# Performance work log

Measured on AMD Instinct MI355X. Metric: run time of the kernel, lower is better.

The kernel has to match this reference:

```python
import jax, jax.numpy as jnp
import numpy as np

VOCAB = 10000
HIDDEN = 256
BATCH = 32
SEQ = 256


def setup_inputs() -> dict:
    key = jax.random.key(0)
    ks = jax.random.split(key, 7)
    s = 1.0 / np.sqrt(HIDDEN)  # torch nn.RNN/Linear init scale
    return {
        "inputs": jax.random.randint(ks[0], (BATCH, SEQ), 0, VOCAB),
        "state": jnp.zeros((1, BATCH, HIDDEN), dtype=jnp.float32),
        "W_ih": jax.random.uniform(ks[1], (HIDDEN, VOCAB), jnp.float32, -s, s),
        "b_ih": jax.random.uniform(ks[2], (HIDDEN,), jnp.float32, -s, s),
        "W_hh": jax.random.uniform(ks[3], (HIDDEN, HIDDEN), jnp.float32, -s, s),
        "b_hh": jax.random.uniform(ks[4], (HIDDEN,), jnp.float32, -s, s),
        "W_out": jax.random.uniform(ks[5], (VOCAB, HIDDEN), jnp.float32, -s, s),
        "b_out": jax.random.uniform(ks[6], (VOCAB,), jnp.float32, -s, s),
    }


def reference(inputs, state, W_ih, b_ih, W_hh, b_hh, W_out, b_out):
    # one_hot(inputs.T) @ W_ih.T is exactly a row-gather of W_ih.T (one-hot
    # entries are exactly 1.0), so gather gives bitwise-identical math.
    # xproj: (seq, batch, hidden)
    xproj = W_ih.T[inputs.T] + b_ih + b_hh

    def step(h, x_t):
        h = jnp.tanh(x_t + h @ W_hh.T)  # (batch, hidden)
        return h, h

    h_last, Y = jax.lax.scan(step, state[0], xproj)  # Y: (seq, batch, hidden)
    logits = Y.reshape(-1, HIDDEN) @ W_out.T + b_out  # (seq*batch, vocab)
    return logits, h_last[None]
```

## Files before the change

kernel.cpp:

```cpp
#include <hip/hip_runtime.h>

#define VOCAB 10000
#define HIDDEN 256
#define BATCH 32
#define SEQ 256
#define NPAD 10112
#define NTILES 79
#define MTILES 64
#define LOGITS_ELEMS 81920000LL

typedef __attribute__((ext_vector_type(8))) short short8;
typedef __attribute__((ext_vector_type(4))) float f32x4;

static __device__ __forceinline__ unsigned short f32_to_bf16(float f) {
    unsigned u = __float_as_uint(f);
    u += 0x7fffu + ((u >> 16) & 1u);
    return (unsigned short)(u >> 16);
}

__global__ __launch_bounds__(256) void transpose_wih(const float* __restrict__ W_ih,
                                                     float* __restrict__ W_ihT) {
    __shared__ float tile[64][65];
    const int v0   = (blockIdx.x >> 2) * 64;
    const int h0   = (blockIdx.x & 3) * 64;
    const int lane = threadIdx.x & 63;
    const int wv   = threadIdx.x >> 6;

#pragma unroll
    for (int i = 0; i < 16; ++i) {
        const int row = i * 4 + wv;
        const int v   = v0 + lane;
        if (v < VOCAB)
            tile[row][lane] = W_ih[(long)(h0 + row) * VOCAB + v];
    }
    __syncthreads();
#pragma unroll
    for (int i = 0; i < 16; ++i) {
        const int vrow = i * 4 + wv;
        const int v    = v0 + vrow;
        if (v < VOCAB)
            W_ihT[(long)v * HIDDEN + h0 + lane] = tile[lane][vrow];
    }
}

__global__ __launch_bounds__(256) void prep_wout(const float* __restrict__ W_out,
                                                 unsigned short* __restrict__ Wb) {
    const int n = blockIdx.x;
    const int k = threadIdx.x;
    float v = (n < VOCAB) ? W_out[(long)n * HIDDEN + k] : 0.f;
    Wb[(long)n * HIDDEN + k] = f32_to_bf16(v);
}

__global__ __launch_bounds__(512, 2) void scan_kernel(
        const int*   __restrict__ inputs,
        const float* __restrict__ state,
        const float* __restrict__ W_hh,
        const float* __restrict__ b_ih,
        const float* __restrict__ b_hh,
        const float* __restrict__ W_ihT,
        unsigned short* __restrict__ Ybf,
        float* __restrict__ hout)
{
    __shared__ float hbuf[HIDDEN];
    __shared__ float psum[4 * HIDDEN];

    const int b  = blockIdx.x;
    const int t  = threadIdx.x;
    const int jj = t & 63;
    const int q  = (t >> 6) & 3;
    const int h2 = t >> 8;

    float w[2][64];
#pragma unroll
    for (int r = 0; r < 2; ++r) {
        const float* src = W_hh + (jj + 64 * (2 * h2 + r)) * HIDDEN + 64 * q;
#pragma unroll
        for (int k4 = 0; k4 < 16; ++k4) {
            const float4 v = *(const float4*)(src + 4 * k4);
            w[r][4 * k4 + 0] = v.x;
            w[r][4 * k4 + 1] = v.y;
            w[r][4 * k4 + 2] = v.z;
            w[r][4 * k4 + 3] = v.w;
        }
    }

    float biasv = 0.f, xcur = 0.f;
    if (t < HIDDEN) {
        biasv   = b_ih[t] + b_hh[t];
        hbuf[t] = state[b * HIDDEN + t];
        const int tok0 = inputs[b * SEQ];
        xcur = W_ihT[(long)tok0 * HIDDEN + t];
    }
    __syncthreads();

    for (int step = 0; step < SEQ; ++step) {
        float xnext = 0.f;
        if (t < HIDDEN && step + 1 < SEQ) {
            const int tokn = inputs[b * SEQ + step + 1];
            xnext = W_ihT[(long)tokn * HIDDEN + t];
        }

        float a00 = 0.f, a01 = 0.f, a10 = 0.f, a11 = 0.f;
#pragma unroll
        for (int k4 = 0; k4 < 8; ++k4) {
            const float4 hv = *(const float4*)&hbuf[64 * q + 4 * k4];
            a00 = fmaf(w[0][4 * k4 + 0], hv.x, a00);
            a00 = fmaf(w[0][4 * k4 + 1], hv.y, a00);
            a00 = fmaf(w[0][4 * k4 + 2], hv.z, a00);
            a00 = fmaf(w[0][4 * k4 + 3], hv.w, a00);
            a10 = fmaf(w[1][4 * k4 + 0], hv.x, a10);
            a10 = fmaf(w[1][4 * k4 + 1], hv.y, a10);
            a10 = fmaf(w[1][4 * k4 + 2], hv.z, a10);
            a10 = fmaf(w[1][4 * k4 + 3], hv.w, a10);
        }
#pragma unroll
        for (int k4 = 8; k4 < 16; ++k4) {
            const float4 hv = *(const float4*)&hbuf[64 * q + 4 * k4];
            a01 = fmaf(w[0][4 * k4 + 0], hv.x, a01);
            a01 = fmaf(w[0][4 * k4 + 1], hv.y, a01);
            a01 = fmaf(w[0][4 * k4 + 2], hv.z, a01);
            a01 = fmaf(w[0][4 * k4 + 3], hv.w, a01);
            a11 = fmaf(w[1][4 * k4 + 0], hv.x, a11);
            a11 = fmaf(w[1][4 * k4 + 1], hv.y, a11);
            a11 = fmaf(w[1][4 * k4 + 2], hv.z, a11);
            a11 = fmaf(w[1][4 * k4 + 3], hv.w, a11);
        }
        psum[q * HIDDEN + jj + 64 * (2 * h2 + 0)] = a00 + a01;
        psum[q * HIDDEN + jj + 64 * (2 * h2 + 1)] = a10 + a11;
        __syncthreads();

        if (t < HIDDEN) {
            const float s = psum[t] + psum[HIDDEN + t]
                          + psum[2 * HIDDEN + t] + psum[3 * HIDDEN + t];
            const float hnew = tanhf(s + xcur + biasv);
            hbuf[t] = hnew;
            Ybf[((long)step * BATCH + b) * HIDDEN + t] = f32_to_bf16(hnew);
            xcur = xnext;
        }
        __syncthreads();
    }

    if (t < HIDDEN) hout[b * HIDDEN + t] = hbuf[t];
}

__global__ __launch_bounds__(256) void gemm_kernel(
        const unsigned short* __restrict__ A,
        const unsigned short* __restrict__ B,
        const float* __restrict__ bias,
        float* __restrict__ C)
{
    __shared__ __align__(16) unsigned short lA[2][128 * 64];
    __shared__ __align__(16) unsigned short lB[2][128 * 64];

    const int t     = threadIdx.x;
    const int bid   = blockIdx.x;
    const int ntile = bid % NTILES;
    const int mtile = bid / NTILES;
    const long m0   = (long)mtile * 128;
    const long n0   = (long)ntile * 128;
    const int lane  = t & 63;
    const int wave  = t >> 6;
    const int wm    = (wave & 1) * 64;
    const int wn    = (wave >> 1) * 64;
    const int l15   = lane & 15;
    const int quad  = lane >> 4;

    const f32x4 zero = {0.f, 0.f, 0.f, 0.f};
    f32x4 acc[4][4];
#pragma unroll
    for (int i = 0; i < 4; ++i)
#pragma unroll
        for (int j = 0; j < 4; ++j)
            acc[i][j] = zero;

    auto stage = [&](int kb, int buf) {
#pragma unroll
        for (int it = 0; it < 4; ++it) {
            const int c   = it * 256 + t;
            const int row = c >> 3;
            const int sk8 = (c & 7) ^ (row & 7);
            const unsigned short* ga = A + (m0 + row) * HIDDEN + kb * 64 + sk8 * 8;
            const unsigned short* gb = B + (n0 + row) * HIDDEN + kb * 64 + sk8 * 8;
            __builtin_amdgcn_global_load_lds(
                (const __attribute__((address_space(1))) void*)ga,
                (__attribute__((address_space(3))) void*)(&lA[buf][c * 8]), 16, 0, 0);
            __builtin_amdgcn_global_load_lds(
                (const __attribute__((address_space(1))) void*)gb,
                (__attribute__((address_space(3))) void*)(&lB[buf][c * 8]), 16, 0, 0);
        }
    };

    stage(0, 0);
    __syncthreads();

#pragma unroll
    for (int kb = 0; kb < 4; ++kb) {
        if (kb < 3) stage(kb + 1, (kb + 1) & 1);
        const unsigned short* bufA = lA[kb & 1];
        const unsigned short* bufB = lB[kb & 1];
#pragma unroll
        for (int ki = 0; ki < 2; ++ki) {
            short8 af[4], bf[4];
#pragma unroll
            for (int i = 0; i < 4; ++i) {
                const int ra = wm + 16 * i + l15;
                af[i] = *(const short8*)
                    &bufA[ra * 64 + (((ki * 4 + quad) ^ (ra & 7)) * 8)];
                const int rb = wn + 16 * i + l15;
                bf[i] = *(const short8*)
                    &bufB[rb * 64 + (((ki * 4 + quad) ^ (rb & 7)) * 8)];
            }
#pragma unroll
            for (int i = 0; i < 4; ++i)
#pragma unroll
                for (int j = 0; j < 4; ++j)
                    acc[i][j] = __builtin_amdgcn_mfma_f32_16x16x32_bf16(
                        af[i], bf[j], acc[i][j], 0, 0, 0);
        }
        if (kb < 3) __syncthreads();
    }

#pragma unroll
    for (int j = 0; j < 4; ++j) {
        const long col = n0 + wn + 16 * j + l15;
        if (col < VOCAB) {
            const float bv = bias[col];
#pragma unroll
            for (int i = 0; i < 4; ++i) {
                const long row = m0 + wm + 16 * i + quad * 4;
                float* Cp = C + row * VOCAB + col;
#pragma unroll
                for (int r = 0; r < 4; ++r)
                    __builtin_nontemporal_store(acc[i][j][r] + bv,
                                                Cp + (long)r * VOCAB);
            }
        }
    }
}

extern "C" void kernel_launch(void* const* d_in, const int* in_sizes, int n_in,
                              void* d_out, int out_size, void* d_ws, size_t ws_size,
                              hipStream_t stream) {
    const int*   inputs = (const int*)  d_in[0];
    const float* state  = (const float*)d_in[1];
    const float* W_ih   = (const float*)d_in[2];
    const float* b_ih   = (const float*)d_in[3];
    const float* W_hh   = (const float*)d_in[4];
    const float* b_hh   = (const float*)d_in[5];
    const float* W_out  = (const float*)d_in[6];
    const float* b_out  = (const float*)d_in[7];
    float* out = (float*)d_out;

    char* ws = (char*)d_ws;
    float*          W_ihT = (float*)ws;
    unsigned short* Wb    = (unsigned short*)(ws + 10240000);
    unsigned short* Ybf   = (unsigned short*)(ws + 15417344);

    transpose_wih<<<157 * 4, 256, 0, stream>>>(W_ih, W_ihT);
    prep_wout<<<NPAD, 256, 0, stream>>>(W_out, Wb);
    scan_kernel<<<BATCH, 512, 0, stream>>>(inputs, state, W_hh, b_ih, b_hh,
                                           W_ihT, Ybf, out + LOGITS_ELEMS);
    gemm_kernel<<<MTILES * NTILES, 256, 0, stream>>>(Ybf, Wb, b_out, out);
}
```

Before: 603.5 us.

## Restructure RNN scan to one barrier per step and merge prep kernels

The scan kernel now assigns each hidden unit to a pair of half-wave lanes that each cover half of K. The two partial sums are combined with a cross-lane shuffle instead of an LDS partial-sum reduction, and the hidden state is double-buffered, so each timestep needs one barrier instead of two. The two weight-prep kernels (W_ih transpose and W_out bf16 conversion) are fused into a single launch to remove one kernel launch. The trade-offs are 128 weight registers per thread and redundant tanh/x loads across lane pairs.

Result: slower. 828.7 us (+37.3%).

```diff
diff --git a/kernel.cpp b/kernel.cpp
--- a/kernel.cpp
+++ b/kernel.cpp
@@ -8,6 +8,8 @@
 #define NTILES 79
 #define MTILES 64
 #define LOGITS_ELEMS 81920000LL
+#define TR_BLOCKS 628
+#define PREP_BLOCKS 707
 
 typedef __attribute__((ext_vector_type(8))) short short8;
 typedef __attribute__((ext_vector_type(4))) float f32x4;
@@ -18,37 +20,41 @@
     return (unsigned short)(u >> 16);
 }
 
-__global__ __launch_bounds__(256) void transpose_wih(const float* __restrict__ W_ih,
-                                                     float* __restrict__ W_ihT) {
+__global__ __launch_bounds__(256) void prep_kernel(const float* __restrict__ W_ih,
+                                                   float* __restrict__ W_ihT,
+                                                   const float* __restrict__ W_out,
+                                                   unsigned short* __restrict__ Wb) {
     __shared__ float tile[64][65];
-    const int v0   = (blockIdx.x >> 2) * 64;
-    const int h0   = (blockIdx.x & 3) * 64;
-    const int lane = threadIdx.x & 63;
-    const int wv   = threadIdx.x >> 6;
-
-#pragma unroll
-    for (int i = 0; i < 16; ++i) {
-        const int row = i * 4 + wv;
-        const int v   = v0 + lane;
-        if (v < VOCAB)
-            tile[row][lane] = W_ih[(long)(h0 + row) * VOCAB + v];
-    }
-    __syncthreads();
-#pragma unroll
-    for (int i = 0; i < 16; ++i) {
-        const int vrow = i * 4 + wv;
-        const int v    = v0 + vrow;
-        if (v < VOCAB)
-            W_ihT[(long)v * HIDDEN + h0 + lane] = tile[lane][vrow];
-    }
-}
-
-__global__ __launch_bounds__(256) void prep_wout(const float* __restrict__ W_out,
-                                                 unsigned short* __restrict__ Wb) {
-    const int n = blockIdx.x;
-    const int k = threadIdx.x;
-    float v = (n < VOCAB) ? W_out[(long)n * HIDDEN + k] : 0.f;
-    Wb[(long)n * HIDDEN + k] = f32_to_bf16(v);
+    const int t = threadIdx.x;
+    if (blockIdx.x < TR_BLOCKS) {
+        const int v0   = (blockIdx.x >> 2) * 64;
+        const int h0   = (blockIdx.x & 3) * 64;
+        const int lane = t & 63;
+        const int wv   = t >> 6;
+#pragma unroll
+        for (int i = 0; i < 16; ++i) {
+            const int row = i * 4 + wv;
+            const int v   = v0 + lane;
+            if (v < VOCAB)
+                tile[row][lane] = W_ih[(long)(h0 + row) * VOCAB + v];
+        }
+        __syncthreads();
+#pragma unroll
+        for (int i = 0; i < 16; ++i) {
+            const int vrow = i * 4 + wv;
+            const int v    = v0 + vrow;
+            if (v < VOCAB)
+                W_ihT[(long)v * HIDDEN + h0 + lane] = tile[lane][vrow];
+        }
+    } else {
+        const int n0 = (blockIdx.x - TR_BLOCKS) * 128;
+#pragma unroll 4
+        for (int r = 0; r < 128; ++r) {
+            const int n = n0 + r;
+            const float v = (n < VOCAB) ? W_out[(long)n * HIDDEN + t] : 0.f;
+            Wb[(long)n * HIDDEN + t] = f32_to_bf16(v);
+        }
+    }
 }
 
 __global__ __launch_bounds__(512, 2) void scan_kernel(
@@ -61,86 +67,83 @@
         unsigned short* __restrict__ Ybf,
         float* __restrict__ hout)
 {
-    __shared__ float hbuf[HIDDEN];
-    __shared__ float psum[4 * HIDDEN];
+    __shared__ float hbuf[2][HIDDEN];
 
     const int b  = blockIdx.x;
     const int t  = threadIdx.x;
-    const int jj = t & 63;
-    const int q  = (t >> 6) & 3;
-    const int h2 = t >> 8;
-
-    float w[2][64];
-#pragma unroll
-    for (int r = 0; r < 2; ++r) {
-        const float* src = W_hh + (jj + 64 * (2 * h2 + r)) * HIDDEN + 64 * q;
-#pragma unroll
-        for (int k4 = 0; k4 < 16; ++k4) {
+    const int wv = t >> 6;
+    const int l  = t & 63;
+    const int l5 = l & 31;
+    const int kh = l >> 5;
+    const int h  = 32 * wv + l5;
+
+    float w[128];
+    {
+        const float* src = W_hh + (long)h * HIDDEN + 128 * kh;
+#pragma unroll
+        for (int k4 = 0; k4 < 32; ++k4) {
             const float4 v = *(const float4*)(src + 4 * k4);
-            w[r][4 * k4 + 0] = v.x;
-            w[r][4 * k4 + 1] = v.y;
-            w[r][4 * k4 + 2] = v.z;
-            w[r][4 * k4 + 3] = v.w;
-        }
-    }
-
-    float biasv = 0.f, xcur = 0.f;
-    if (t < HIDDEN) {
-        biasv   = b_ih[t] + b_hh[t];
-        hbuf[t] = state[b * HIDDEN + t];
-        const int tok0 = inputs[b * SEQ];
-        xcur = W_ihT[(long)tok0 * HIDDEN + t];
-    }
+            w[4 * k4 + 0] = v.x;
+            w[4 * k4 + 1] = v.y;
+            w[4 * k4 + 2] = v.z;
+            w[4 * k4 + 3] = v.w;
+        }
+    }
+
+    const float biasv = b_ih[h] + b_hh[h];
+    if (l < 32) hbuf[0][h] = state[b * HIDDEN + h];
+    const int tok0 = inputs[b * SEQ];
+    float xcur = W_ihT[(long)tok0 * HIDDEN + h];
     __syncthreads();
 
+    int cur = 0;
     for (int step = 0; step < SEQ; ++step) {
         float xnext = 0.f;
-        if (t < HIDDEN && step + 1 < SEQ) {
+        if (step + 1 < SEQ) {
             const int tokn = inputs[b * SEQ + step + 1];
-            xnext = W_ihT[(long)tokn * HIDDEN + t];
-        }
-
-        float a00 = 0.f, a01 = 0.f, a10 = 0.f, a11 = 0.f;
-#pragma unroll
-        for (int k4 = 0; k4 < 8; ++k4) {
-            const float4 hv = *(const float4*)&hbuf[64 * q + 4 * k4];
-            a00 = fmaf(w[0][4 * k4 + 0], hv.x, a00);
-            a00 = fmaf(w[0][4 * k4 + 1], hv.y, a00);
-            a00 = fmaf(w[0][4 * k4 + 2], hv.z, a00);
-            a00 = fmaf(w[0][4 * k4 + 3], hv.w, a00);
-            a10 = fmaf(w[1][4 * k4 + 0], hv.x, a10);
-            a10 = fmaf(w[1][4 * k4 + 1], hv.y, a10);
-            a10 = fmaf(w[1][4 * k4 + 2], hv.z, a10);
-            a10 = fmaf(w[1][4 * k4 + 3], hv.w, a10);
-        }
-#pragma unroll
-        for (int k4 = 8; k4 < 16; ++k4) {
-            const float4 hv = *(const float4*)&hbuf[64 * q + 4 * k4];
-            a01 = fmaf(w[0][4 * k4 + 0], hv.x, a01);
-            a01 = fmaf(w[0][4 * k4 + 1], hv.y, a01);
-            a01 = fmaf(w[0][4 * k4 + 2], hv.z, a01);
-            a01 = fmaf(w[0][4 * k4 + 3], hv.w, a01);
-            a11 = fmaf(w[1][4 * k4 + 0], hv.x, a11);
-            a11 = fmaf(w[1][4 * k4 + 1], hv.y, a11);
-            a11 = fmaf(w[1][4 * k4 + 2], hv.z, a11);
-            a11 = fmaf(w[1][4 * k4 + 3], hv.w, a11);
-        }
-        psum[q * HIDDEN + jj + 64 * (2 * h2 + 0)] = a00 + a01;
-        psum[q * HIDDEN + jj + 64 * (2 * h2 + 1)] = a10 + a11;
+            xnext = W_ihT[(long)tokn * HIDDEN + h];
+        }
+
+        float a0 = 0.f, a1 = 0.f, a2 = 0.f, a3 = 0.f;
+        const float* hb = &hbuf[cur][128 * kh];
+#pragma unroll
+        for (int k16 = 0; k16 < 8; ++k16) {
+            const float4 h0 = *(const float4*)(hb + 16 * k16 + 0);
+            const float4 h1 = *(const float4*)(hb + 16 * k16 + 4);
+            const float4 h2 = *(const float4*)(hb + 16 * k16 + 8);
+            const float4 h3 = *(const float4*)(hb + 16 * k16 + 12);
+            const int kb = 16 * k16;
+            a0 = fmaf(w[kb +  0], h0.x, a0);
+            a0 = fmaf(w[kb +  1], h0.y, a0);
+            a0 = fmaf(w[kb +  2], h0.z, a0);
+            a0 = fmaf(w[kb +  3], h0.w, a0);
+            a1 = fmaf(w[kb +  4], h1.x, a1);
+            a1 = fmaf(w[kb +  5], h1.y, a1);
+            a1 = fmaf(w[kb +  6], h1.z, a1);
+            a1 = fmaf(w[kb +  7], h1.w, a1);
+            a2 = fmaf(w[kb +  8], h2.x, a2);
+            a2 = fmaf(w[kb +  9], h2.y, a2);
+            a2 = fmaf(w[kb + 10], h2.z, a2);
+            a2 = fmaf(w[kb + 11], h2.w, a2);
+            a3 = fmaf(w[kb + 12], h3.x, a3);
+            a3 = fmaf(w[kb + 13], h3.y, a3);
+            a3 = fmaf(w[kb + 14], h3.z, a3);
+            a3 = fmaf(w[kb + 15], h3.w, a3);
+        }
+        float s = (a0 + a1) + (a2 + a3);
+        s += __shfl_xor(s, 32);
+
+        const float hnew = tanhf(s + xcur + biasv);
+        if (l < 32) {
+            hbuf[cur ^ 1][h] = hnew;
+            Ybf[((long)step * BATCH + b) * HIDDEN + h] = f32_to_bf16(hnew);
+        }
+        xcur = xnext;
+        cur ^= 1;
         __syncthreads();
-
-        if (t < HIDDEN) {
-            const float s = psum[t] + psum[HIDDEN + t]
-                          + psum[2 * HIDDEN + t] + psum[3 * HIDDEN + t];
-            const float hnew = tanhf(s + xcur + biasv);
-            hbuf[t] = hnew;
-            Ybf[((long)step * BATCH + b) * HIDDEN + t] = f32_to_bf16(hnew);
-            xcur = xnext;
-        }
-        __syncthreads();
-    }
-
-    if (t < HIDDEN) hout[b * HIDDEN + t] = hbuf[t];
+    }
+
+    if (l < 32) hout[b * HIDDEN + h] = hbuf[cur][h];
 }
 
 __global__ __launch_bounds__(256) void gemm_kernel(
@@ -256,8 +259,7 @@
     unsigned short* Wb    = (unsigned short*)(ws + 10240000);
     unsigned short* Ybf   = (unsigned short*)(ws + 15417344);
 
-    transpose_wih<<<157 * 4, 256, 0, stream>>>(W_ih, W_ihT);
-    prep_wout<<<NPAD, 256, 0, stream>>>(W_out, Wb);
+    prep_kernel<<<PREP_BLOCKS, 256, 0, stream>>>(W_ih, W_ihT, W_out, Wb);
     scan_kernel<<<BATCH, 512, 0, stream>>>(inputs, state, W_hh, b_ih, b_hh,
                                            W_ihT, Ybf, out + LOGITS_ELEMS);
     gemm_kernel<<<MTILES * NTILES, 256, 0, stream>>>(Ybf, Wb, b_out, out);
```
